# Optimization experiments

Measured on AMD Instinct MI355X. Metric: run time of the kernel, lower is better.

Reference implementation:

```python
import jax, jax.numpy as jnp
import numpy as np

N = 50000
E = 800000
D_IN = 256
H1 = 512   # hidden_channels
H2 = 256   # out_channels == hidden_dim
NUM_CLASSES = 5
NEG_SLOPE = 0.2


def _edge_softmax(logits, dst, n):
    # numerically-stable softmax over edges grouped by destination node
    m = jax.ops.segment_max(logits, dst, num_segments=n)
    e = jnp.exp(logits - m[dst])
    s = jax.ops.segment_sum(e, dst, num_segments=n)
    return e / (s[dst] + 1e-16)


def _gat_conv(x, src, dst, W, att_src, att_dst, bias):
    h = x @ W                                   # [N, C] (PyG lin_src, no bias)
    a_s = (h * att_src).sum(-1)                 # [N]
    a_d = (h * att_dst).sum(-1)                 # [N]
    logits = jax.nn.leaky_relu(a_s[src] + a_d[dst], NEG_SLOPE)  # [E]
    alpha = _edge_softmax(logits, dst, x.shape[0])              # [E]
    out = jax.ops.segment_sum(h[src] * alpha[:, None], dst, num_segments=x.shape[0])
    return out + bias


def setup_inputs() -> dict:
    key = jax.random.key(0)
    ks = jax.random.split(key, 20)
    g = lambda k, shp, fan: jax.random.normal(k, shp, jnp.float32) * (1.0 / np.sqrt(fan))
    inp = {
        "x": jax.random.normal(ks[0], (N, D_IN), jnp.float32),
        "edge_index": jax.random.randint(ks[1], (2, E), 0, N, jnp.int64),
        # conv1 (GATConv, heads=1)
        "W1": g(ks[2], (D_IN, H1), D_IN),
        "att_src1": g(ks[3], (H1,), H1),
        "att_dst1": g(ks[4], (H1,), H1),
        "b_conv1": jnp.zeros((H1,), jnp.float32),
        # lin1 (dense residual)
        "A1": g(ks[5], (D_IN, H1), D_IN),
        "b1": jnp.zeros((H1,), jnp.float32),
        # conv2
        "W2": g(ks[6], (H1, H2), H1),
        "att_src2": g(ks[7], (H2,), H2),
        "att_dst2": g(ks[8], (H2,), H2),
        "b_conv2": jnp.zeros((H2,), jnp.float32),
        # lin2
        "A2": g(ks[9], (H1, H2), H1),
        "b2": jnp.zeros((H2,), jnp.float32),
        # 3 hidden MLP layers [256 -> 256]
        "Hw1": g(ks[10], (H2, H2), H2), "Hb1": jnp.zeros((H2,), jnp.float32),
        "Hw2": g(ks[11], (H2, H2), H2), "Hb2": jnp.zeros((H2,), jnp.float32),
        "Hw3": g(ks[12], (H2, H2), H2), "Hb3": jnp.zeros((H2,), jnp.float32),
        # classifier
        "fcw": g(ks[13], (H2, NUM_CLASSES), H2),
        "fcb": jnp.zeros((NUM_CLASSES,), jnp.float32),
    }
    return inp


def reference(x, edge_index, W1, att_src1, att_dst1, b_conv1, A1, b1,
              W2, att_src2, att_dst2, b_conv2, A2, b2,
              Hw1, Hb1, Hw2, Hb2, Hw3, Hb3, fcw, fcb):
    src, dst = edge_index[0], edge_index[1]
    h = _gat_conv(x, src, dst, W1, att_src1, att_dst1, b_conv1) + (x @ A1 + b1)
    h = jax.nn.relu(h)
    h = _gat_conv(h, src, dst, W2, att_src2, att_dst2, b_conv2) + (h @ A2 + b2)
    for w, b in ((Hw1, Hb1), (Hw2, Hb2), (Hw3, Hb3)):
        h = jax.nn.relu(h @ w + b)
    logits = h @ fcw + fcb
    return jax.nn.softmax(logits, axis=-1)
```

## Files before the change

### kernel.cpp

```cpp
#include <hip/hip_runtime.h>

typedef unsigned short u16;
typedef short short8 __attribute__((ext_vector_type(8)));
typedef u16 u16x4 __attribute__((ext_vector_type(4)));
typedef u16 u16x8 __attribute__((ext_vector_type(8)));
typedef float float4v __attribute__((ext_vector_type(4)));

#define NEG_SLOPE 0.2f

static __device__ __forceinline__ float b2f(u16 u) {
    union { unsigned int i; float f; } x; x.i = ((unsigned int)u) << 16; return x.f;
}
static __device__ __forceinline__ u16 f2b(float f) {
    unsigned int u = __float_as_uint(f);
    unsigned int r = (u + 0x7fffu + ((u >> 16) & 1u)) >> 16;
    return (u16)r;
}

__global__ void k_diag(float* out, int n, float val)
{
    int i = blockIdx.x * 256 + threadIdx.x;
    if (i < n) out[i] = val;
}

__global__ void scan_csr(const int* off, const int* srcs, int N, int E,
                         int* flag, int bit)
{
    int i = blockIdx.x * 256 + threadIdx.x;
    if (i < N) {
        int a = off[i], b = off[i + 1];
        if (a < 0 || b < a || b > E) atomicOr(flag, bit);
    }
    if (i == 0 && off[N] != E) atomicOr(flag, bit);
    if (i < E) {
        if ((unsigned)srcs[i] >= (unsigned)N) atomicOr(flag, bit);
    }
}

__global__ void k_final_diag(const int* flag, float* out, int n)
{
    int f = *flag;
    if (f == 0) return;
    int b = __ffs(f) - 1;
    float val = 32.0f * (b + 1);
    int i = blockIdx.x * 256 + threadIdx.x;
    if (i < n) out[i] = val;
}

__global__ void k_detect(const int* ei, int E, int* flag64)
{
    __shared__ int zc;
    if (threadIdx.x == 0) zc = 0;
    __syncthreads();
    int idx = 1 + 2 * (int)threadIdx.x;
    int z = (idx < 2 * E && ei[idx] == 0) ? 1 : 0;
    atomicAdd(&zc, z);
    __syncthreads();
    if (threadIdx.x == 0) *flag64 = (zc >= 200) ? 1 : 0;
}

__global__ void k_extract(const int* ei, int E, const int* flag64,
                          int* src, int* dst, int* deg, int N)
{
    int e = blockIdx.x * 256 + threadIdx.x;
    if (e >= E) return;
    int s, d;
    if (*flag64) {
        s = ei[2 * e];
        d = ei[2 * E + 2 * e];
    } else {
        s = ei[e];
        d = ei[E + e];
    }
    src[e] = s; dst[e] = d;
    if ((unsigned)d < (unsigned)N) atomicAdd(&deg[d], 1);
}

__global__ __launch_bounds__(256)
void k_scan_a(const int* __restrict__ deg, int* __restrict__ off,
              int* __restrict__ partial, int N)
{
    __shared__ int sd[256];
    int tid = threadIdx.x;
    int base = blockIdx.x * 1024;
    int i0 = base + tid * 4;
    int v0 = 0, v1 = 0, v2 = 0, v3 = 0;
    if (i0 < N)     v0 = deg[i0];
    if (i0 + 1 < N) v1 = deg[i0 + 1];
    if (i0 + 2 < N) v2 = deg[i0 + 2];
    if (i0 + 3 < N) v3 = deg[i0 + 3];
    int t = v0 + v1 + v2 + v3;
    sd[tid] = t;
    __syncthreads();
    #pragma unroll
    for (int s = 1; s < 256; s <<= 1) {
        int u = (tid >= s) ? sd[tid - s] : 0;
        __syncthreads();
        sd[tid] += u;
        __syncthreads();
    }
    int excl = sd[tid] - t;
    if (i0 < N)     off[i0]     = excl;
    if (i0 + 1 < N) off[i0 + 1] = excl + v0;
    if (i0 + 2 < N) off[i0 + 2] = excl + v0 + v1;
    if (i0 + 3 < N) off[i0 + 3] = excl + v0 + v1 + v2;
    if (tid == 255) partial[blockIdx.x] = sd[255];
}

__global__ __launch_bounds__(1024)
void k_scan_b(int* partial, int nblk)
{
    __shared__ int sd[1024];
    __shared__ int running;
    int tid = threadIdx.x;
    if (tid == 0) running = 0;
    __syncthreads();
    for (int base = 0; base < nblk; base += 1024) {
        int i = base + tid;
        int v = (i < nblk) ? partial[i] : 0;
        sd[tid] = v;
        __syncthreads();
        for (int s = 1; s < 1024; s <<= 1) {
            int u = (tid >= s) ? sd[tid - s] : 0;
            __syncthreads();
            sd[tid] += u;
            __syncthreads();
        }
        if (i < nblk) partial[i] = sd[tid] - v + running;
        int total = sd[1023];
        __syncthreads();
        if (tid == 0) running += total;
        __syncthreads();
    }
}

__global__ __launch_bounds__(256)
void k_scan_c(int* __restrict__ off, int* __restrict__ cursor,
              const int* __restrict__ partial, int N, int E)
{
    int i = blockIdx.x * 256 + threadIdx.x;
    if (i < N) {
        int v = off[i] + partial[i >> 10];
        off[i] = v;
        cursor[i] = v;
    }
    if (i == 0) off[N] = E;
}

__global__ void k_scatter(const int* src, const int* dst, int* cursor,
                          int* srcs, int E, int N)
{
    int e = blockIdx.x * 256 + threadIdx.x;
    if (e < E) {
        int d = dst[e];
        if ((unsigned)d < (unsigned)N) {
            int p = atomicAdd(&cursor[d], 1);
            if ((unsigned)p < (unsigned)E) srcs[p] = src[e];
        }
    }
}

__global__ __launch_bounds__(256)
void k_castdot(const float* __restrict__ x, const float* __restrict__ vs,
               const float* __restrict__ vd, u16* __restrict__ xb,
               float* __restrict__ a_s, float* __restrict__ a_d, int N)
{
    int tid = threadIdx.x;
    int rowb = tid >> 5;
    int col8 = (tid & 31) * 8;
    int n = blockIdx.x * 8 + rowb;
    if (n >= N) return;
    const float* xr = x + (size_t)n * 256 + col8;
    float4 v0 = *(const float4*)xr;
    float4 v1 = *(const float4*)(xr + 4);
    int4 w;
    w.x = (int)f2b(v0.x) | ((int)f2b(v0.y) << 16);
    w.y = (int)f2b(v0.z) | ((int)f2b(v0.w) << 16);
    w.z = (int)f2b(v1.x) | ((int)f2b(v1.y) << 16);
    w.w = (int)f2b(v1.z) | ((int)f2b(v1.w) << 16);
    *(int4*)(xb + (size_t)n * 256 + col8) = w;

    float4 s0 = *(const float4*)(vs + col8);
    float4 s1 = *(const float4*)(vs + col8 + 4);
    float4 d0 = *(const float4*)(vd + col8);
    float4 d1 = *(const float4*)(vd + col8 + 4);
    float ss = v0.x*s0.x + v0.y*s0.y + v0.z*s0.z + v0.w*s0.w
             + v1.x*s1.x + v1.y*s1.y + v1.z*s1.z + v1.w*s1.w;
    float sd = v0.x*d0.x + v0.y*d0.y + v0.z*d0.z + v0.w*d0.w
             + v1.x*d1.x + v1.y*d1.y + v1.z*d1.z + v1.w*d1.w;
    #pragma unroll
    for (int m = 16; m; m >>= 1) {
        ss += __shfl_xor(ss, m, 64);
        sd += __shfl_xor(sd, m, 64);
    }
    if ((tid & 31) == 0) { a_s[n] = ss; a_d[n] = sd; }
}

__global__ __launch_bounds__(64)
void k_packAll(const float* A1w, const float* W1, const float* W2, const float* A2w,
               const float* Hw1, const float* Hw2, const float* Hw3,
               u16* WT1, u16* WT2, u16* WTH)
{
    int z = blockIdx.z;
    const float *in1, *in2; int ksplit, csplit, in_ld, NC16; u16* out;
    if (z == 0)      { in1 = A1w; in2 = W1;  ksplit = 256; csplit = 0;   in_ld = 512; out = WT1; NC16 = 32; }
    else if (z == 1) { in1 = W2;  in2 = A2w; ksplit = 0;   csplit = 256; in_ld = 256; out = WT2; NC16 = 32; }
    else {
        if (blockIdx.x >= 16 || blockIdx.y >= 8) return;
        in1 = (z == 2) ? Hw1 : (z == 3) ? Hw2 : Hw3;
        in2 = nullptr; ksplit = 0; csplit = 0; in_ld = 256; NC16 = 16;
        out = WTH + (size_t)(z - 2) * 65536;
    }
    int l = threadIdx.x;
    int cf = blockIdx.x, kt = blockIdx.y;
    int col = cf * 16 + (l & 15);
    int kbase = kt * 32 + (l >> 4) * 8;
    const float* src = in1;
    int cc = col, koff = 0;
    if (ksplit > 0 && kbase >= ksplit) { src = in2; koff = ksplit; }
    if (csplit > 0 && col >= csplit)   { src = in2; cc = col - csplit; }
    u16* o = out + ((size_t)(kt * NC16 + cf) * 512) + l * 8;
    #pragma unroll
    for (int j = 0; j < 8; ++j)
        o[j] = f2b(src[(size_t)(kbase - koff + j) * in_ld + cc]);
}

__global__ __launch_bounds__(256)
void k_rowdot2f(const float* __restrict__ A, int ld, int H,
                const float* __restrict__ vs, const float* __restrict__ vd,
                float* a_s, float* a_d, int N)
{
    int wave = threadIdx.x >> 6, lane = threadIdx.x & 63;
    int n = blockIdx.x * 4 + wave;
    if (n >= N) return;
    const float* ar = A + (size_t)n * ld;
    float ss = 0.f, sd = 0.f;
    for (int i = lane * 4; i < H; i += 256) {
        float4 v  = *(const float4*)(ar + i);
        float4 s4 = *(const float4*)(vs + i);
        float4 d4 = *(const float4*)(vd + i);
        ss += v.x * s4.x + v.y * s4.y + v.z * s4.z + v.w * s4.w;
        sd += v.x * d4.x + v.y * d4.y + v.z * d4.z + v.w * d4.w;
    }
    #pragma unroll
    for (int m = 32; m; m >>= 1) {
        ss += __shfl_xor(ss, m, 64);
        sd += __shfl_xor(sd, m, 64);
    }
    if (lane == 0) { a_s[n] = ss; a_d[n] = sd; }
}

__global__ __launch_bounds__(256)
void k_rowdot2(const u16* h, int ld, int H, const float* vs, const float* vd,
               float* a_s, float* a_d, int N)
{
    int wave = threadIdx.x >> 6, lane = threadIdx.x & 63;
    int n = blockIdx.x * 4 + wave;
    if (n >= N) return;
    const u16* hr = h + (size_t)n * ld;
    float ss = 0.f, sd = 0.f;
    for (int i = lane; i < H; i += 64) {
        float v = b2f(hr[i]);
        ss += v * vs[i];
        sd += v * vd[i];
    }
    #pragma unroll
    for (int m = 32; m; m >>= 1) {
        ss += __shfl_xor(ss, m, 64);
        sd += __shfl_xor(sd, m, 64);
    }
    if (lane == 0) { a_s[n] = ss; a_d[n] = sd; }
}

__global__ __launch_bounds__(256)
void k_alpha(const int* __restrict__ off, const int* __restrict__ srcs,
             const float* __restrict__ a_s, const float* __restrict__ a_d,
             float* __restrict__ alpha, int N)
{
    int wave = threadIdx.x >> 6, lane = threadIdx.x & 63;
    int n = blockIdx.x * 4 + wave;
    if (n >= N) return;
    int base = off[n], end = off[n + 1];
    float adn = a_d[n];
    float m = -1e30f, s = 0.f;
    for (int p = base + lane; p < end; p += 64) {
        int sx = srcs[p];
        sx = ((unsigned)sx < (unsigned)N) ? sx : 0;
        float z = a_s[sx] + adn;
        z = fmaxf(z, NEG_SLOPE * z);
        float mn = fmaxf(m, z);
        s = s * __expf(m - mn) + __expf(z - mn);
        m = mn;
    }
    #pragma unroll
    for (int msk = 32; msk; msk >>= 1) {
        float mo = __shfl_xor(m, msk, 64);
        float so = __shfl_xor(s, msk, 64);
        float mn = fmaxf(m, mo);
        s = s * __expf(m - mn) + so * __expf(mo - mn);
        m = mn;
    }
    float inv = 1.f / (s + 1e-16f);
    for (int p = base + lane; p < end; p += 64) {
        int sx = srcs[p];
        sx = ((unsigned)sx < (unsigned)N) ? sx : 0;
        float z = a_s[sx] + adn;
        z = fmaxf(z, NEG_SLOPE * z);
        alpha[p] = __expf(z - m) * inv;
    }
}

__global__ __launch_bounds__(256)
void k_aggw(const u16* __restrict__ rows, const int* __restrict__ off,
            const int* __restrict__ srcs, const float* __restrict__ alpha,
            const u16* __restrict__ add, u16* __restrict__ out, int N)
{
    int wave = threadIdx.x >> 6, lane = threadIdx.x & 63;
    int n = blockIdx.x * 4 + wave;
    if (n >= N) return;
    int base = off[n], end = off[n + 1];
    int half = lane >> 5;
    int c8 = (lane & 31) * 8;
    float acc[8] = {};
    int p = base;
    for (; p + 3 < end; p += 4) {
        int sA = srcs[p + half];
        int sB = srcs[p + 2 + half];
        sA = ((unsigned)sA < (unsigned)N) ? sA : 0;
        sB = ((unsigned)sB < (unsigned)N) ? sB : 0;
        float wA = alpha[p + half];
        float wB = alpha[p + 2 + half];
        u16x8 vA = *(const u16x8*)(rows + (size_t)sA * 256 + c8);
        u16x8 vB = *(const u16x8*)(rows + (size_t)sB * 256 + c8);
        #pragma unroll
        for (int j = 0; j < 8; ++j)
            acc[j] += wA * b2f(vA[j]) + wB * b2f(vB[j]);
    }
    for (; p + 1 < end; p += 2) {
        int sA = srcs[p + half];
        sA = ((unsigned)sA < (unsigned)N) ? sA : 0;
        float wA = alpha[p + half];
        u16x8 vA = *(const u16x8*)(rows + (size_t)sA * 256 + c8);
        #pragma unroll
        for (int j = 0; j < 8; ++j)
            acc[j] += wA * b2f(vA[j]);
    }
    if (p < end) {
        int sA = srcs[p];
        sA = ((unsigned)sA < (unsigned)N) ? sA : 0;
        float wA = half ? 0.f : alpha[p];
        u16x8 vA = *(const u16x8*)(rows + (size_t)sA * 256 + c8);
        #pragma unroll
        for (int j = 0; j < 8; ++j)
            acc[j] += wA * b2f(vA[j]);
    }
    #pragma unroll
    for (int j = 0; j < 8; ++j)
        acc[j] += __shfl_xor(acc[j], 32, 64);
    if (half == 0) {
        size_t ob = (size_t)n * 256 + c8;
        if (add) {
            u16x8 ad8 = *(const u16x8*)(add + ob);
            #pragma unroll
            for (int j = 0; j < 8; ++j) acc[j] += b2f(ad8[j]);
        }
        u16x8 o;
        #pragma unroll
        for (int j = 0; j < 8; ++j) o[j] = f2b(acc[j]);
        *(u16x8*)(out + ob) = o;
    }
}

__global__ __launch_bounds__(512)
void bigfull(const u16* __restrict__ A1, int lda1,
             const u16* __restrict__ A2, int lda2,
             const u16* __restrict__ WTf,
             const float* b0a, const float* b0b,
             const float* b1a, const float* b1b,
             u16* C1, int ldc1, u16* C2, int ldc2,
             int M, int relu0, int relu1)
{
    __shared__ u16 As[64 * 32];

    const int tid = threadIdx.x;
    const int w = tid >> 6, lane = tid & 63;
    const int m16 = lane & 15, q = lane >> 4;
    const int rowBase = blockIdx.x * 64;

    float4v acc[16] = {};

    for (int k0 = 0; k0 < 512; k0 += 32) {
        const int kt = k0 >> 5;
        __syncthreads();
        if (tid < 256) {
            int rf = tid >> 6, al = tid & 63;
            int grow = rowBase + rf * 16 + (al & 15);
            if (grow >= M) grow = M - 1;
            int kk = k0 + (al >> 4) * 8;
            const u16* src = (kk < 256)
                ? A1 + (size_t)grow * lda1 + kk
                : A2 + (size_t)grow * lda2 + (kk - 256);
            *(int4*)&As[tid * 8] = *(const int4*)src;
        }
        __syncthreads();

        short8 a[4], b[4];
        #pragma unroll
        for (int c = 0; c < 4; ++c) {
            int4 bv = *(const int4*)(WTf + (size_t)kt * 16384
                                     + (size_t)(w * 4 + c) * 512 + lane * 8);
            b[c] = *(short8*)&bv;
        }
        #pragma unroll
        for (int r = 0; r < 4; ++r)
            a[r] = *(const short8*)&As[r * 512 + lane * 8];
        #pragma unroll
        for (int r = 0; r < 4; ++r)
            #pragma unroll
            for (int c = 0; c < 4; ++c)
                acc[r * 4 + c] = __builtin_amdgcn_mfma_f32_16x16x32_bf16(
                    a[r], b[c], acc[r * 4 + c], 0, 0, 0);
    }

    const int colgrp = w >> 2;
    const float* ba = colgrp ? b1a : b0a;
    const float* bb = colgrp ? b1b : b0b;
    u16* C  = colgrp ? C2 : C1;
    const int ldc  = colgrp ? ldc2 : ldc1;
    const int relu = colgrp ? relu1 : relu0;
    #pragma unroll
    for (int c = 0; c < 4; ++c) {
        int lc = ((w & 3) * 4 + c) * 16 + m16;
        float bv = (ba ? ba[lc] : 0.f) + (bb ? bb[lc] : 0.f);
        #pragma unroll
        for (int r = 0; r < 4; ++r)
            #pragma unroll
            for (int i = 0; i < 4; ++i) {
                int grow = rowBase + r * 16 + q * 4 + i;
                if (grow < M) {
                    float v = acc[r * 4 + c][i] + bv;
                    if (relu) v = fmaxf(v, 0.f);
                    C[(size_t)grow * ldc + lc] = f2b(v);
                }
            }
    }
}

__global__ __launch_bounds__(256)
void k_mlp3fc(const u16* __restrict__ WTHf,
              const float* Hb1, const float* Hb2, const float* Hb3,
              const float* __restrict__ fcw, const float* __restrict__ fcb,
              const u16* __restrict__ Hin, float* __restrict__ out, int M)
{
    __shared__ u16 P[64 * 256];

    const int tid = threadIdx.x;
    const int w = tid >> 6, lane = tid & 63;
    const int m16 = lane & 15, q = lane >> 4;
    const int rowBase = blockIdx.x * 64;

    #pragma unroll
    for (int p = 0; p < 8; ++p) {
        int ch = p * 256 + tid;
        int f = ch >> 6, l = ch & 63;
        int kt = f >> 2, rf = f & 3;
        int grow = rowBase + rf * 16 + (l & 15);
        if (grow >= M) grow = M - 1;
        int col = kt * 32 + (l >> 4) * 8;
        *(int4*)&P[ch * 8] = *(const int4*)(Hin + (size_t)grow * 256 + col);
    }
    __syncthreads();

    const float* biases[3] = {Hb1, Hb2, Hb3};
    for (int L = 0; L < 3; ++L) {
        const u16* WTf = WTHf + (size_t)L * 65536;
        float4v acc[16] = {};
        #pragma unroll 2
        for (int kt = 0; kt < 8; ++kt) {
            short8 a[4], b[4];
            #pragma unroll
            for (int c = 0; c < 4; ++c) {
                int4 bv = *(const int4*)(WTf + (size_t)(kt * 16 + w * 4 + c) * 512
                                         + lane * 8);
                b[c] = *(short8*)&bv;
            }
            #pragma unroll
            for (int r = 0; r < 4; ++r)
                a[r] = *(const short8*)&P[(kt * 4 + r) * 512 + lane * 8];
            #pragma unroll
            for (int r = 0; r < 4; ++r)
                #pragma unroll
                for (int c = 0; c < 4; ++c)
                    acc[r * 4 + c] = __builtin_amdgcn_mfma_f32_16x16x32_bf16(
                        a[r], b[c], acc[r * 4 + c], 0, 0, 0);
        }
        const float* bias = biases[L];
        __syncthreads();
        #pragma unroll
        for (int c = 0; c < 4; ++c) {
            int col = w * 64 + c * 16 + m16;
            float bv = bias[col];
            int kt2 = col >> 5;
            int l2h = 16 * ((col & 31) >> 3);
            int j2 = col & 7;
            #pragma unroll
            for (int r = 0; r < 4; ++r)
                #pragma unroll
                for (int i = 0; i < 4; ++i) {
                    int l2 = (q * 4 + i) + l2h;
                    P[(size_t)(kt2 * 4 + r) * 512 + l2 * 8 + j2] =
                        f2b(fmaxf(acc[r * 4 + c][i] + bv, 0.f));
                }
        }
        __syncthreads();
    }

    float p5[5] = {0.f, 0.f, 0.f, 0.f, 0.f};
    #pragma unroll
    for (int kt = 0; kt < 8; ++kt) {
        u16x8 v = *(const u16x8*)&P[(kt * 4 + w) * 512 + lane * 8];
        int colb = kt * 32 + q * 8;
        #pragma unroll
        for (int j = 0; j < 8; ++j) {
            float hv = b2f(v[j]);
            const float* wr = fcw + (size_t)(colb + j) * 5;
            #pragma unroll
            for (int c = 0; c < 5; ++c) p5[c] += hv * wr[c];
        }
    }
    #pragma unroll
    for (int c = 0; c < 5; ++c) {
        p5[c] += __shfl_xor(p5[c], 16, 64);
        p5[c] += __shfl_xor(p5[c], 32, 64);
    }
    int grow = rowBase + w * 16 + m16;
    if (q == 0 && grow < M) {
        float mx = -1e30f;
        #pragma unroll
        for (int c = 0; c < 5; ++c) { p5[c] += fcb[c]; mx = fmaxf(mx, p5[c]); }
        float s = 0.f, e[5];
        #pragma unroll
        for (int c = 0; c < 5; ++c) { e[c] = __expf(p5[c] - mx); s += e[c]; }
        float inv = 1.f / s;
        #pragma unroll
        for (int c = 0; c < 5; ++c) out[(size_t)grow * 5 + c] = e[c] * inv;
    }
}

extern "C" void kernel_launch(void* const* d_in, const int* in_sizes, int n_in,
                              void* d_out, int out_size, void* d_ws, size_t ws_size,
                              hipStream_t stream)
{
    const float* x    = (const float*)d_in[0];
    const int*   ei   = (const int*)  d_in[1];
    const float* W1   = (const float*)d_in[2];
    const float* as1  = (const float*)d_in[3];
    const float* ad1  = (const float*)d_in[4];
    const float* bc1  = (const float*)d_in[5];
    const float* A1w  = (const float*)d_in[6];
    const float* b1   = (const float*)d_in[7];
    const float* W2   = (const float*)d_in[8];
    const float* as2  = (const float*)d_in[9];
    const float* ad2  = (const float*)d_in[10];
    const float* bc2  = (const float*)d_in[11];
    const float* A2w  = (const float*)d_in[12];
    const float* b2   = (const float*)d_in[13];
    const float* Hw1  = (const float*)d_in[14];
    const float* Hb1  = (const float*)d_in[15];
    const float* Hw2  = (const float*)d_in[16];
    const float* Hb2  = (const float*)d_in[17];
    const float* Hw3  = (const float*)d_in[18];
    const float* Hb3  = (const float*)d_in[19];
    const float* fcw  = (const float*)d_in[20];
    const float* fcb  = (const float*)d_in[21];
    float* out = (float*)d_out;

    const int D = 256;
    const int N = in_sizes[0] / D;
    const int E = in_sizes[1] / 2;

    char* w = (char*)d_ws;
    auto alloc = [&](size_t bytes) {
        char* p = w;
        w += (bytes + 255) & ~(size_t)255;
        return p;
    };
    int*   flag   = (int*)  alloc(256);
    int*   flag64 = (int*)  alloc(256);
    float* a_s    = (float*)alloc((size_t)N * 4);
    float* a_d    = (float*)alloc((size_t)N * 4);
    float* vs1    = (float*)alloc(1024);
    float* vd1    = (float*)alloc(1024);
    int*   deg    = (int*)  alloc((size_t)N * 4);
    int*   cursor = (int*)  alloc((size_t)N * 4);
    int*   offA   = (int*)  alloc((size_t)(N + 1) * 4);
    int*   part   = (int*)  alloc((size_t)((N + 1023) / 1024 + 1) * 4);
    int*   srcs   = (int*)  alloc((size_t)E * 4);
    float* alpha  = (float*)alloc((size_t)E * 4);
    u16*   WT1    = (u16*)  alloc(512 * 512 * 2);
    u16*   WT2    = (u16*)  alloc(512 * 512 * 2);
    u16*   WTH    = (u16*)  alloc(3 * 256 * 256 * 2);
    u16*   BUF1   = (u16*)  alloc((size_t)N * 512 * 2);
    u16*   BUF2   = (u16*)  alloc((size_t)N * 512 * 2);

    int* src32 = (int*)BUF1;
    int* dst32 = src32 + E;

    size_t need = (size_t)(w - (char*)d_ws);
    if (ws_size < need) {
        float code = 1000.0f + (float)(ws_size >> 20);
        k_diag<<<(out_size + 255) / 256, 256, 0, stream>>>(out, out_size, code);
        return;
    }

    const int EB  = (E + 255) / 256;
    const int NB4 = (N + 3) / 4;
    const int OB  = (out_size + 255) / 256;
    const int NE  = (N > E ? N : E);
    const int RB64 = (N + 63) / 64;
    const int NBLK = (N + 1023) / 1024;
    const size_t NH2 = (size_t)N * 256;
    u16* XB   = BUF1;
    u16* AGGX = BUF1 + NH2;

    hipMemsetAsync(flag, 0, 4, stream);
    hipMemsetAsync(deg, 0, (size_t)N * 4, stream);

    k_detect <<<1, 256, 0, stream>>>(ei, E, flag64);
    k_extract<<<EB, 256, 0, stream>>>(ei, E, flag64, src32, dst32, deg, N);
    k_scan_a <<<NBLK, 256, 0, stream>>>(deg, offA, part, N);
    k_scan_b <<<1, 1024, 0, stream>>>(part, NBLK);
    k_scan_c <<<(N + 255) / 256, 256, 0, stream>>>(offA, cursor, part, N, E);
    k_scatter<<<EB, 256, 0, stream>>>(src32, dst32, cursor, srcs, E, N);
    scan_csr <<<(NE + 255) / 256, 256, 0, stream>>>(offA, srcs, N, E, flag, 1);

    k_packAll<<<dim3(32, 16, 5), 64, 0, stream>>>(A1w, W1, W2, A2w,
                                                  Hw1, Hw2, Hw3, WT1, WT2, WTH);

    k_rowdot2f<<<64, 256, 0, stream>>>(W1, 512, 512, as1, ad1, vs1, vd1, 256);
    k_castdot<<<(N + 7) / 8, 256, 0, stream>>>(x, vs1, vd1, XB, a_s, a_d, N);
    k_alpha<<<NB4, 256, 0, stream>>>(offA, srcs, a_s, a_d, alpha, N);

    k_aggw<<<NB4, 256, 0, stream>>>(XB, offA, srcs, alpha, nullptr, AGGX, N);

    bigfull<<<RB64, 512, 0, stream>>>(XB, 256, AGGX, 256, WT1,
                                      b1, bc1, b1 + 256, bc1 + 256,
                                      BUF2, 512, BUF2 + 256, 512, N, 1, 1);

    bigfull<<<RB64, 512, 0, stream>>>(BUF2, 512, BUF2 + 256, 512, WT2,
                                      nullptr, nullptr, b2, bc2,
                                      BUF1, 256, BUF1 + NH2, 256, N, 0, 0);

    k_rowdot2<<<NB4, 256, 0, stream>>>(BUF1, 256, 256, as2, ad2, a_s, a_d, N);
    k_alpha<<<NB4, 256, 0, stream>>>(offA, srcs, a_s, a_d, alpha, N);
    k_aggw<<<NB4, 256, 0, stream>>>(BUF1, offA, srcs, alpha, BUF1 + NH2, BUF2, N);

    k_mlp3fc<<<RB64, 256, 0, stream>>>(WTH, Hb1, Hb2, Hb3, fcw, fcb,
                                       BUF2, out, N);

    k_final_diag<<<OB, 256, 0, stream>>>(flag, out, out_size);
}
```

Before: 572.4 us.

## Fuse conv2 attention dot products into GEMM epilogue; widen MLP kernel to 512 threads

The separate rowdot kernel for the second GAT layer's attention scores is removed. The second bigfull GEMM now computes the per-row dot products with att_src/att_dst from its bf16-rounded accumulators in the epilogue and accumulates them into a_s/a_d with atomics, after a memset zeroes those buffers. Separately, the fused MLP+classifier kernel moves from 256 to 512 threads, halving the per-wave column tiles and accumulators, with only 4 waves doing the final classifier. This saves one pass over BUF1 and a launch, at the cost of atomics, extra memsets and a changed reduction order.

```diff
diff --git a/kernel.cpp b/kernel.cpp
--- a/kernel.cpp
+++ b/kernel.cpp
@@ -241,28 +241,6 @@
         float4 d4 = *(const float4*)(vd + i);
         ss += v.x * s4.x + v.y * s4.y + v.z * s4.z + v.w * s4.w;
         sd += v.x * d4.x + v.y * d4.y + v.z * d4.z + v.w * d4.w;
-    }
-    #pragma unroll
-    for (int m = 32; m; m >>= 1) {
-        ss += __shfl_xor(ss, m, 64);
-        sd += __shfl_xor(sd, m, 64);
-    }
-    if (lane == 0) { a_s[n] = ss; a_d[n] = sd; }
-}
-
-__global__ __launch_bounds__(256)
-void k_rowdot2(const u16* h, int ld, int H, const float* vs, const float* vd,
-               float* a_s, float* a_d, int N)
-{
-    int wave = threadIdx.x >> 6, lane = threadIdx.x & 63;
-    int n = blockIdx.x * 4 + wave;
-    if (n >= N) return;
-    const u16* hr = h + (size_t)n * ld;
-    float ss = 0.f, sd = 0.f;
-    for (int i = lane; i < H; i += 64) {
-        float v = b2f(hr[i]);
-        ss += v * vs[i];
-        sd += v * vd[i];
     }
     #pragma unroll
     for (int m = 32; m; m >>= 1) {
@@ -378,6 +356,8 @@
              const float* b0a, const float* b0b,
              const float* b1a, const float* b1b,
              u16* C1, int ldc1, u16* C2, int ldc2,
+             const float* __restrict__ dotS, const float* __restrict__ dotD,
+             float* oaS, float* oaD,
              int M, int relu0, int relu1)
 {
     __shared__ u16 As[64 * 32];
@@ -444,9 +424,35 @@
                 }
             }
     }
-}
-
-__global__ __launch_bounds__(256)
+
+    if (dotS && colgrp == 0) {
+        #pragma unroll
+        for (int r = 0; r < 4; ++r)
+            #pragma unroll
+            for (int i = 0; i < 4; ++i) {
+                float ss = 0.f, sd = 0.f;
+                #pragma unroll
+                for (int c = 0; c < 4; ++c) {
+                    int lc = ((w & 3) * 4 + c) * 16 + m16;
+                    float v = b2f(f2b(acc[r * 4 + c][i]));
+                    ss += v * dotS[lc];
+                    sd += v * dotD[lc];
+                }
+                #pragma unroll
+                for (int msk = 1; msk < 16; msk <<= 1) {
+                    ss += __shfl_xor(ss, msk, 64);
+                    sd += __shfl_xor(sd, msk, 64);
+                }
+                int grow = rowBase + r * 16 + q * 4 + i;
+                if (m16 == 0 && grow < M) {
+                    atomicAdd(&oaS[grow], ss);
+                    atomicAdd(&oaD[grow], sd);
+                }
+            }
+    }
+}
+
+__global__ __launch_bounds__(512)
 void k_mlp3fc(const u16* __restrict__ WTHf,
               const float* Hb1, const float* Hb2, const float* Hb3,
               const float* __restrict__ fcw, const float* __restrict__ fcb,
@@ -460,8 +466,8 @@
     const int rowBase = blockIdx.x * 64;
 
     #pragma unroll
-    for (int p = 0; p < 8; ++p) {
-        int ch = p * 256 + tid;
+    for (int p = 0; p < 4; ++p) {
+        int ch = p * 512 + tid;
         int f = ch >> 6, l = ch & 63;
         int kt = f >> 2, rf = f & 3;
         int grow = rowBase + rf * 16 + (l & 15);
@@ -474,13 +480,13 @@
     const float* biases[3] = {Hb1, Hb2, Hb3};
     for (int L = 0; L < 3; ++L) {
         const u16* WTf = WTHf + (size_t)L * 65536;
-        float4v acc[16] = {};
+        float4v acc[8] = {};
         #pragma unroll 2
         for (int kt = 0; kt < 8; ++kt) {
-            short8 a[4], b[4];
-            #pragma unroll
-            for (int c = 0; c < 4; ++c) {
-                int4 bv = *(const int4*)(WTf + (size_t)(kt * 16 + w * 4 + c) * 512
+            short8 a[4], b[2];
+            #pragma unroll
+            for (int c = 0; c < 2; ++c) {
+                int4 bv = *(const int4*)(WTf + (size_t)(kt * 16 + w * 2 + c) * 512
                                          + lane * 8);
                 b[c] = *(short8*)&bv;
             }
@@ -490,15 +496,15 @@
             #pragma unroll
             for (int r = 0; r < 4; ++r)
                 #pragma unroll
-                for (int c = 0; c < 4; ++c)
-                    acc[r * 4 + c] = __builtin_amdgcn_mfma_f32_16x16x32_bf16(
-                        a[r], b[c], acc[r * 4 + c], 0, 0, 0);
+                for (int c = 0; c < 2; ++c)
+                    acc[r * 2 + c] = __builtin_amdgcn_mfma_f32_16x16x32_bf16(
+                        a[r], b[c], acc[r * 2 + c], 0, 0, 0);
         }
         const float* bias = biases[L];
         __syncthreads();
         #pragma unroll
-        for (int c = 0; c < 4; ++c) {
-            int col = w * 64 + c * 16 + m16;
+        for (int c = 0; c < 2; ++c) {
+            int col = w * 32 + c * 16 + m16;
             float bv = bias[col];
             int kt2 = col >> 5;
             int l2h = 16 * ((col & 31) >> 3);
@@ -509,41 +515,43 @@
                 for (int i = 0; i < 4; ++i) {
                     int l2 = (q * 4 + i) + l2h;
                     P[(size_t)(kt2 * 4 + r) * 512 + l2 * 8 + j2] =
-                        f2b(fmaxf(acc[r * 4 + c][i] + bv, 0.f));
+                        f2b(fmaxf(acc[r * 2 + c][i] + bv, 0.f));
                 }
         }
         __syncthreads();
     }
 
-    float p5[5] = {0.f, 0.f, 0.f, 0.f, 0.f};
-    #pragma unroll
-    for (int kt = 0; kt < 8; ++kt) {
-        u16x8 v = *(const u16x8*)&P[(kt * 4 + w) * 512 + lane * 8];
-        int colb = kt * 32 + q * 8;
-        #pragma unroll
-        for (int j = 0; j < 8; ++j) {
-            float hv = b2f(v[j]);
-            const float* wr = fcw + (size_t)(colb + j) * 5;
-            #pragma unroll
-            for (int c = 0; c < 5; ++c) p5[c] += hv * wr[c];
-        }
-    }
-    #pragma unroll
-    for (int c = 0; c < 5; ++c) {
-        p5[c] += __shfl_xor(p5[c], 16, 64);
-        p5[c] += __shfl_xor(p5[c], 32, 64);
-    }
-    int grow = rowBase + w * 16 + m16;
-    if (q == 0 && grow < M) {
-        float mx = -1e30f;
-        #pragma unroll
-        for (int c = 0; c < 5; ++c) { p5[c] += fcb[c]; mx = fmaxf(mx, p5[c]); }
-        float s = 0.f, e[5];
-        #pragma unroll
-        for (int c = 0; c < 5; ++c) { e[c] = __expf(p5[c] - mx); s += e[c]; }
-        float inv = 1.f / s;
-        #pragma unroll
-        for (int c = 0; c < 5; ++c) out[(size_t)grow * 5 + c] = e[c] * inv;
+    if (w < 4) {
+        float p5[5] = {0.f, 0.f, 0.f, 0.f, 0.f};
+        #pragma unroll
+        for (int kt = 0; kt < 8; ++kt) {
+            u16x8 v = *(const u16x8*)&P[(kt * 4 + w) * 512 + lane * 8];
+            int colb = kt * 32 + q * 8;
+            #pragma unroll
+            for (int j = 0; j < 8; ++j) {
+                float hv = b2f(v[j]);
+                const float* wr = fcw + (size_t)(colb + j) * 5;
+                #pragma unroll
+                for (int c = 0; c < 5; ++c) p5[c] += hv * wr[c];
+            }
+        }
+        #pragma unroll
+        for (int c = 0; c < 5; ++c) {
+            p5[c] += __shfl_xor(p5[c], 16, 64);
+            p5[c] += __shfl_xor(p5[c], 32, 64);
+        }
+        int grow = rowBase + w * 16 + m16;
+        if (q == 0 && grow < M) {
+            float mx = -1e30f;
+            #pragma unroll
+            for (int c = 0; c < 5; ++c) { p5[c] += fcb[c]; mx = fmaxf(mx, p5[c]); }
+            float s = 0.f, e[5];
+            #pragma unroll
+            for (int c = 0; c < 5; ++c) { e[c] = __expf(p5[c] - mx); s += e[c]; }
+            float inv = 1.f / s;
+            #pragma unroll
+            for (int c = 0; c < 5; ++c) out[(size_t)grow * 5 + c] = e[c] * inv;
+        }
     }
 }
 
@@ -641,21 +649,27 @@
     k_castdot<<<(N + 7) / 8, 256, 0, stream>>>(x, vs1, vd1, XB, a_s, a_d, N);
     k_alpha<<<NB4, 256, 0, stream>>>(offA, srcs, a_s, a_d, alpha, N);
 
+    hipMemsetAsync(a_s, 0, (size_t)N * 4, stream);
+    hipMemsetAsync(a_d, 0, (size_t)N * 4, stream);
+
     k_aggw<<<NB4, 256, 0, stream>>>(XB, offA, srcs, alpha, nullptr, AGGX, N);
 
     bigfull<<<RB64, 512, 0, stream>>>(XB, 256, AGGX, 256, WT1,
                                       b1, bc1, b1 + 256, bc1 + 256,
-                                      BUF2, 512, BUF2 + 256, 512, N, 1, 1);
+                                      BUF2, 512, BUF2 + 256, 512,
+                                      nullptr, nullptr, nullptr, nullptr,
+                                      N, 1, 1);
 
     bigfull<<<RB64, 512, 0, stream>>>(BUF2, 512, BUF2 + 256, 512, WT2,
                                       nullptr, nullptr, b2, bc2,
-                                      BUF1, 256, BUF1 + NH2, 256, N, 0, 0);
-
-    k_rowdot2<<<NB4, 256, 0, stream>>>(BUF1, 256, 256, as2, ad2, a_s, a_d, N);
+                                      BUF1, 256, BUF1 + NH2, 256,
+                                      as2, ad2, a_s, a_d,
+                                      N, 0, 0);
+
     k_alpha<<<NB4, 256, 0, stream>>>(offA, srcs, a_s, a_d, alpha, N);
     k_aggw<<<NB4, 256, 0, stream>>>(BUF1, offA, srcs, alpha, BUF1 + NH2, BUF2, N);
 
-    k_mlp3fc<<<RB64, 256, 0, stream>>>(WTH, Hb1, Hb2, Hb3, fcw, fcb,
+    k_mlp3fc<<<RB64, 512, 0, stream>>>(WTH, Hb1, Hb2, Hb3, fcw, fcb,
                                        BUF2, out, N);
 
     k_final_diag<<<OB, 256, 0, stream>>>(flag, out, out_size);
```

New measurement: 543.6 us. -5.0%, faster.
